# Optimization experiments

Hardware: AMD Instinct MI355X
Metric: run time of the kernel (lower is better)

## Reference

```python
import jax, jax.numpy as jnp
import numpy as np

NUM_HEADS = 8
NORM_GROUPS = 32
EPS = 1e-5


def setup_inputs() -> dict:
    key = jax.random.key(0)
    k1, k2, k3 = jax.random.split(key, 3)
    b, c, h, w = 16, 256, 64, 64
    x = jax.random.normal(k1, (b, c, h, w), dtype=jnp.float32)
    gn_w = jnp.ones((c,), dtype=jnp.float32)
    gn_b = jnp.zeros((c,), dtype=jnp.float32)
    # 1x1 convs == channel matmuls; init like torch (kaiming-ish scale)
    w_qkv = jax.random.normal(k2, (3 * c, c), dtype=jnp.float32) / np.sqrt(c)
    w_proj = jax.random.normal(k3, (c, c), dtype=jnp.float32) / np.sqrt(c)
    b_proj = jnp.zeros((c,), dtype=jnp.float32)
    return {"x": x, "gn_w": gn_w, "gn_b": gn_b, "w_qkv": w_qkv,
            "w_proj": w_proj, "b_proj": b_proj}


def reference(x, gn_w, gn_b, w_qkv, w_proj, b_proj):
    b, c, h, w = x.shape
    H = NUM_HEADS
    d = c // H
    n = h * w
    # GroupNorm over (channels_per_group, h, w)
    xg = x.reshape(b, NORM_GROUPS, -1)
    mu = jnp.mean(xg, axis=-1, keepdims=True)
    var = jnp.mean(jnp.square(xg - mu), axis=-1, keepdims=True)
    xn = ((xg - mu) * jax.lax.rsqrt(var + EPS)).reshape(b, c, h, w)
    xn = xn * gn_w[None, :, None, None] + gn_b[None, :, None, None]
    # 1x1 conv -> (b, 3c, h, w); channel layout is (qkv, heads, d)
    qkv = jnp.einsum('oc,bchw->bohw', w_qkv, xn)
    qkv = qkv.reshape(b, 3, H, d, n)
    q, k, v = qkv[:, 0], qkv[:, 1], qkv[:, 2]  # each (b, H, d, n)
    k = jax.nn.softmax(k, axis=-1)
    # linear attention: small (d x d) state per head
    att = jnp.einsum('bhdn,bhen->bhde', k, v)
    out = jnp.einsum('bhde,bhdn->bhen', att, q)  # (b, H, d, n)
    out = out.reshape(b, c, h, w)
    return jnp.einsum('oc,bchw->bohw', w_proj, out) + b_proj[None, :, None, None]
```

## Files before the change

kernel.cpp:

```cpp
#include <hip/hip_runtime.h>
#include <stdint.h>

#define BATCH 16
#define CCH   256
#define NSP   4096
#define QKV_M 768

typedef unsigned short u16;
typedef short  short8 __attribute__((ext_vector_type(8)));
typedef float  f32x4  __attribute__((ext_vector_type(4)));

__device__ __forceinline__ float bf2f(u16 h) {
  union { unsigned int u; float f; } x; x.u = ((unsigned int)h) << 16; return x.f;
}
__device__ __forceinline__ u16 f2bf(float f) {
  union { float f; unsigned int u; } x; x.f = f;
  unsigned int r = 0x7fffu + ((x.u >> 16) & 1u);
  return (u16)((x.u + r) >> 16);
}

#define GLB(p) ((__attribute__((address_space(1))) void*)(p))
#define LDSP(p) ((__attribute__((address_space(3))) void*)(p))

__global__ __launch_bounds__(256) void convw_kernel(const float* __restrict__ wq,
                                                    const float* __restrict__ wp,
                                                    u16* __restrict__ dst) {
  const int i = (blockIdx.x * 256 + threadIdx.x) * 4;
  float4 v = (i < 196608) ? *(const float4*)(wq + i)
                          : *(const float4*)(wp + (i - 196608));
  ushort4 o;
  o.x = f2bf(v.x); o.y = f2bf(v.y); o.z = f2bf(v.z); o.w = f2bf(v.w);
  *(ushort4*)(dst + i) = o;
}

__global__ __launch_bounds__(256) void gn_stats(const float* __restrict__ x,
                                                float2* __restrict__ stats,
                                                float* __restrict__ att4) {
  const int blk = blockIdx.x;
  const int tid = threadIdx.x;
  {
    float* az = att4 + (size_t)blk * 264;
    for (int i = tid; i < 264; i += 256) az[i] = 0.f;
  }
  const float4* xv = (const float4*)(x + (size_t)blk * 32768);
  float s = 0.f, ss = 0.f;
  for (int i = tid; i < 8192; i += 256) {
    float4 u = xv[i];
    s  += u.x + u.y + u.z + u.w;
    ss += u.x * u.x + u.y * u.y + u.z * u.z + u.w * u.w;
  }
#pragma unroll
  for (int off = 32; off > 0; off >>= 1) {
    s  += __shfl_down(s, off);
    ss += __shfl_down(ss, off);
  }
  __shared__ float red[8];
  const int wave = tid >> 6, lane = tid & 63;
  if (lane == 0) { red[wave * 2] = s; red[wave * 2 + 1] = ss; }
  __syncthreads();
  if (tid == 0) {
    const float S  = red[0] + red[2] + red[4] + red[6];
    const float SS = red[1] + red[3] + red[5] + red[7];
    const float mean = S * (1.f / 32768.f);
    const float var  = SS * (1.f / 32768.f) - mean * mean;
    stats[blk] = make_float2(mean, rsqrtf(var + 1e-5f));
  }
}

__global__ __launch_bounds__(256) void gn_apply_t(const float* __restrict__ x,
                                                  const float* __restrict__ gw,
                                                  const float* __restrict__ gb,
                                                  const float2* __restrict__ stats,
                                                  u16* __restrict__ xnT) {
  __shared__ u16 ls[64][72];
  const int b = blockIdx.z, c0 = blockIdx.y * 64, n0 = blockIdx.x * 64;
  const int tid = threadIdx.x;
#pragma unroll
  for (int r = 0; r < 4; ++r) {
    const int cc = (tid >> 4) + r * 16;
    const int nn = (tid & 15) * 4;
    const int c = c0 + cc;
    const float2 st = stats[b * 32 + (c >> 3)];
    const float wv = gw[c] * st.y;
    const float bv = gb[c] - st.x * wv;
    float4 u = *(const float4*)(x + ((size_t)b * CCH + c) * NSP + n0 + nn);
    ushort4 o;
    o.x = f2bf(u.x * wv + bv);
    o.y = f2bf(u.y * wv + bv);
    o.z = f2bf(u.z * wv + bv);
    o.w = f2bf(u.w * wv + bv);
    *(ushort4*)&ls[cc][nn] = o;
  }
  __syncthreads();
#pragma unroll
  for (int p = 0; p < 2; ++p) {
    const int idx = tid + p * 256;
    const int nn = idx >> 3;
    const int cb = (idx & 7) * 8;
    u16 tmp[8];
#pragma unroll
    for (int j = 0; j < 8; ++j) tmp[j] = ls[cb + j][nn];
    *(uint4*)(xnT + ((size_t)b * NSP + n0 + nn) * CCH + c0 + cb) = *(uint4*)tmp;
  }
}

template <int OUTF32, int TRQ>
__global__ __launch_bounds__(256) void gemm_mfma(const u16* __restrict__ A,
                                                 const u16* __restrict__ Bt,
                                                 const float* __restrict__ bias,
                                                 void* __restrict__ Cm, int M,
                                                 int aBatch, long btStride) {
  __shared__ __align__(16) u16 smem[17408];
  const int tid = threadIdx.x, wave = tid >> 6, lane = tid & 63;
  const int n0 = blockIdx.x * 128, m0 = blockIdx.y * 128, bz = blockIdx.z;
  const u16* Ab = A + (size_t)bz * aBatch;
  const u16* Bb = Bt + (size_t)bz * btStride;

  const int lrow = lane >> 3;
  const int kcl  = ((lane & 7) ^ lrow) * 8;
  const u16* pA[4]; const u16* pB[4];
#pragma unroll
  for (int j = 0; j < 4; ++j) {
    const int row = j * 32 + wave * 8 + lrow;
    pA[j] = Ab + (size_t)(m0 + row) * CCH + kcl;
    pB[j] = Bb + (size_t)(n0 + row) * CCH + kcl;
  }
  u16* lA = smem;
  u16* lB = smem + 8192;

  const int wm = wave >> 1, wn = wave & 1;
  f32x4 acc[4][4];
#pragma unroll
  for (int i = 0; i < 4; ++i)
#pragma unroll
    for (int j = 0; j < 4; ++j) acc[i][j] = (f32x4){0.f, 0.f, 0.f, 0.f};

  for (int it = 0; it < 4; ++it) {
#pragma unroll
    for (int j = 0; j < 4; ++j) {
      __builtin_amdgcn_global_load_lds(GLB(pA[j]), LDSP(lA + (j * 256 + wave * 64) * 8), 16, 0, 0);
      __builtin_amdgcn_global_load_lds(GLB(pB[j]), LDSP(lB + (j * 256 + wave * 64) * 8), 16, 0, 0);
      pA[j] += 64; pB[j] += 64;
    }
    __syncthreads();
#pragma unroll
    for (int w = 0; w < 2; ++w) {
      const int kcf = w * 4 + (lane >> 4);
      short8 af[4], bfr[4];
#pragma unroll
      for (int mt = 0; mt < 4; ++mt) {
        const int row = wm * 64 + mt * 16 + (lane & 15);
        af[mt] = *(const short8*)&lA[(row * 8 + (kcf ^ (row & 7))) * 8];
      }
#pragma unroll
      for (int nt = 0; nt < 4; ++nt) {
        const int row = wn * 64 + nt * 16 + (lane & 15);
        bfr[nt] = *(const short8*)&lB[(row * 8 + (kcf ^ (row & 7))) * 8];
      }
#pragma unroll
      for (int mt = 0; mt < 4; ++mt)
#pragma unroll
        for (int nt = 0; nt < 4; ++nt)
          acc[mt][nt] = __builtin_amdgcn_mfma_f32_16x16x32_bf16(af[mt], bfr[nt], acc[mt][nt], 0, 0, 0);
    }
    __syncthreads();
  }

  if (!OUTF32) {
    u16* cl = smem;
    const bool tr = TRQ && (m0 < 256);
#pragma unroll
    for (int mt = 0; mt < 4; ++mt)
#pragma unroll
      for (int nt = 0; nt < 4; ++nt)
#pragma unroll
        for (int r = 0; r < 4; ++r) {
          const int row = wm * 64 + mt * 16 + (lane >> 4) * 4 + r;
          const int col = wn * 64 + nt * 16 + (lane & 15);
          if (tr) cl[col * 136 + row] = f2bf(acc[mt][nt][r]);
          else    cl[row * 136 + col] = f2bf(acc[mt][nt][r]);
        }
    __syncthreads();
    u16* C = (u16*)Cm + (size_t)bz * M * NSP;
    if (tr) {
#pragma unroll
      for (int j = 0; j < 8; ++j) {
        const int idx = tid + j * 256;
        const int nl = idx >> 4, mc = (idx & 15) * 8;
        *(uint4*)(C + (size_t)(n0 + nl) * CCH + m0 + mc) =
            *(const uint4*)&cl[nl * 136 + mc];
      }
    } else {
#pragma unroll
      for (int j = 0; j < 8; ++j) {
        const int idx = tid + j * 256;
        const int row = idx >> 4, chunk = idx & 15;
        *(uint4*)(C + (size_t)(m0 + row) * NSP + n0 + chunk * 8) =
            *(const uint4*)&cl[row * 136 + chunk * 8];
      }
    }
  } else {
    float* clf = (float*)smem;
    float* C = (float*)Cm + (size_t)bz * M * NSP;
#pragma unroll
    for (int pass = 0; pass < 2; ++pass) {
      if (wm == pass) {
#pragma unroll
        for (int mt = 0; mt < 4; ++mt)
#pragma unroll
          for (int nt = 0; nt < 4; ++nt)
#pragma unroll
            for (int r = 0; r < 4; ++r) {
              const int rl = mt * 16 + (lane >> 4) * 4 + r;
              const int col = wn * 64 + nt * 16 + (lane & 15);
              clf[rl * 132 + col] = acc[mt][nt][r] + bias[m0 + pass * 64 + rl];
            }
      }
      __syncthreads();
#pragma unroll
      for (int j = 0; j < 8; ++j) {
        const int idx = tid + j * 256;
        const int row = idx >> 5, chunk = idx & 31;
        *(float4*)(C + (size_t)(m0 + pass * 64 + row) * NSP + n0 + chunk * 4) =
            *(const float4*)&clf[row * 132 + chunk * 4];
      }
      __syncthreads();
    }
  }
}

__global__ __launch_bounds__(256, 4) void att2_kernel(const u16* __restrict__ qkv,
                                                      float* __restrict__ att4) {
  const int b = blockIdx.z, h = blockIdx.y;
  const int bh = b * 8 + h;
  const int tid = threadIdx.x, wave = tid >> 6, lane = tid & 63;
  const int n0 = blockIdx.x * 512 + wave * 128;
  const u16* kp = qkv + ((size_t)b * QKV_M + 256 + h * 32) * NSP;
  const u16* vp = qkv + ((size_t)b * QKV_M + 512 + h * 32) * NSP;
  const int r  = lane & 15;
  const int kc = (lane >> 4) * 8;

  f32x4 acc[2][2], accl[2];
#pragma unroll
  for (int i = 0; i < 2; ++i) {
    accl[i] = (f32x4){0.f, 0.f, 0.f, 0.f};
#pragma unroll
    for (int j = 0; j < 2; ++j) acc[i][j] = (f32x4){0.f, 0.f, 0.f, 0.f};
  }
  short8 ones;
#pragma unroll
  for (int j = 0; j < 8; ++j) ones[j] = (short)0x3F80;

  const size_t base0 = (size_t)r * NSP + (size_t)(n0 + kc);
#pragma unroll
  for (int c = 0; c < 4; ++c) {
    const size_t off = base0 + (size_t)c * 32;
    short8 k0 = *(const short8*)(kp + off);
    short8 k1 = *(const short8*)(kp + off + (size_t)16 * NSP);
    short8 v0 = *(const short8*)(vp + off);
    short8 v1 = *(const short8*)(vp + off + (size_t)16 * NSP);
    short8 e0, e1;
#pragma unroll
    for (int j = 0; j < 8; ++j) {
      e0[j] = (short)f2bf(__expf(bf2f((u16)k0[j])));
      e1[j] = (short)f2bf(__expf(bf2f((u16)k1[j])));
    }
    acc[0][0] = __builtin_amdgcn_mfma_f32_16x16x32_bf16(e0, v0, acc[0][0], 0, 0, 0);
    acc[0][1] = __builtin_amdgcn_mfma_f32_16x16x32_bf16(e0, v1, acc[0][1], 0, 0, 0);
    acc[1][0] = __builtin_amdgcn_mfma_f32_16x16x32_bf16(e1, v0, acc[1][0], 0, 0, 0);
    acc[1][1] = __builtin_amdgcn_mfma_f32_16x16x32_bf16(e1, v1, acc[1][1], 0, 0, 0);
    accl[0]   = __builtin_amdgcn_mfma_f32_16x16x32_bf16(e0, ones, accl[0], 0, 0, 0);
    accl[1]   = __builtin_amdgcn_mfma_f32_16x16x32_bf16(e1, ones, accl[1], 0, 0, 0);
  }

  __shared__ float ratt[4][32][34];
  __shared__ float rl[4][32];
  const int rq = lane >> 4;
#pragma unroll
  for (int dt = 0; dt < 2; ++dt) {
#pragma unroll
    for (int et = 0; et < 2; ++et)
#pragma unroll
      for (int j = 0; j < 4; ++j)
        ratt[wave][dt * 16 + rq * 4 + j][et * 16 + r] = acc[dt][et][j];
    if (r == 0)
#pragma unroll
      for (int j = 0; j < 4; ++j) rl[wave][dt * 16 + rq * 4 + j] = accl[dt][j];
  }
  __syncthreads();
  float* ap = att4 + (size_t)bh * 1056;
  for (int i = tid; i < 1024; i += 256) {
    const int d = i >> 5, e = i & 31;
    atomicAdd(&ap[i], ratt[0][d][e] + ratt[1][d][e] + ratt[2][d][e] + ratt[3][d][e]);
  }
  if (tid < 32)
    atomicAdd(&ap[1024 + tid], rl[0][tid] + rl[1][tid] + rl[2][tid] + rl[3][tid]);
}

__global__ __launch_bounds__(256) void w2_kernel(const u16* __restrict__ wp_bf,
                                                 const float* __restrict__ att4,
                                                 u16* __restrict__ W2) {
  const int b = blockIdx.x >> 4;
  const int o0 = (blockIdx.x & 15) * 16;
  const int tid = threadIdx.x;
  const int h = tid >> 5, d = tid & 31;
  const float* ap = att4 + ((size_t)b * 8 + h) * 1056;
  const float linv = 1.f / ap[1024 + d];
  float as[32];
#pragma unroll
  for (int e = 0; e < 32; ++e) as[e] = ap[d * 32 + e] * linv;
  u16* w2p = W2 + (size_t)b * 65536;
  for (int oi = 0; oi < 16; ++oi) {
    const int o = o0 + oi;
    const uint4* wr = (const uint4*)(wp_bf + o * 256 + h * 32);
    float acc = 0.f;
#pragma unroll
    for (int j = 0; j < 4; ++j) {
      uint4 u = wr[j];
      const u16* w8 = (const u16*)&u;
#pragma unroll
      for (int t = 0; t < 8; ++t) acc += bf2f(w8[t]) * as[j * 8 + t];
    }
    w2p[o * 256 + tid] = f2bf(acc);
  }
}

extern "C" void kernel_launch(void* const* d_in, const int* in_sizes, int n_in,
                              void* d_out, int out_size, void* d_ws, size_t ws_size,
                              hipStream_t stream) {
  const float* x      = (const float*)d_in[0];
  const float* gn_w   = (const float*)d_in[1];
  const float* gn_b   = (const float*)d_in[2];
  const float* w_qkv  = (const float*)d_in[3];
  const float* w_proj = (const float*)d_in[4];
  const float* b_proj = (const float*)d_in[5];
  float* out = (float*)d_out;

  char* ws = (char*)d_ws;
  u16*    xnT   = (u16*)ws;
  u16*    qkv   = (u16*)(ws + 33554432ull);
  float*  att4  = (float*)(ws + 134217728ull);
  float2* stats = (float2*)(ws + 134758400ull);
  u16*    wbf   = (u16*)(ws + 134762496ull);
  u16* wq_bf = wbf;
  u16* wp_bf = wbf + 196608;
  u16* W2 = xnT;

  convw_kernel<<<256, 256, 0, stream>>>(w_qkv, w_proj, wbf);
  gn_stats<<<512, 256, 0, stream>>>(x, stats, att4);
  gn_apply_t<<<dim3(64, 4, 16), 256, 0, stream>>>(x, gn_w, gn_b, stats, xnT);
  gemm_mfma<0, 1><<<dim3(32, 6, 16), 256, 0, stream>>>(wq_bf, xnT, nullptr, qkv,
                                                       QKV_M, 0, (long)NSP * CCH);
  att2_kernel<<<dim3(8, 8, 16), 256, 0, stream>>>(qkv, att4);
  w2_kernel<<<256, 256, 0, stream>>>(wp_bf, att4, W2);
  gemm_mfma<1, 0><<<dim3(32, 2, 16), 256, 0, stream>>>(W2, qkv, b_proj, out,
                                                       CCH, 65536, (long)QKV_M * NSP);
}
```

Before: 234.3 us.

## Fuse K/V projection GEMM with linear-attention state accumulation

The QKV GEMM now computes only the Q rows, and a new kernel computes the K and V tiles per 128-column block directly from the normalized input. It applies exp to K, keeps both tiles in LDS, and accumulates the per-head K·V^T and softmax denominators into att4 with atomics. This avoids writing K and V to global memory and reading them back in a separate pass. In exchange, each block issues many more global atomics (32 column blocks per head instead of 8), and LDS use grows to about 68KB per block, which may lower occupancy.

```diff
diff --git a/kernel.cpp b/kernel.cpp
--- a/kernel.cpp
+++ b/kernel.cpp
@@ -229,72 +229,126 @@
   }
 }
 
-__global__ __launch_bounds__(256, 4) void att2_kernel(const u16* __restrict__ qkv,
-                                                      float* __restrict__ att4) {
-  const int b = blockIdx.z, h = blockIdx.y;
-  const int bh = b * 8 + h;
+__global__ __launch_bounds__(256) void gemm_kv_att(const u16* __restrict__ A,
+                                                   const u16* __restrict__ Bt,
+                                                   float* __restrict__ att4) {
+  __shared__ __align__(16) u16 smem[34816];
   const int tid = threadIdx.x, wave = tid >> 6, lane = tid & 63;
-  const int n0 = blockIdx.x * 512 + wave * 128;
-  const u16* kp = qkv + ((size_t)b * QKV_M + 256 + h * 32) * NSP;
-  const u16* vp = qkv + ((size_t)b * QKV_M + 512 + h * 32) * NSP;
-  const int r  = lane & 15;
-  const int kc = (lane >> 4) * 8;
-
-  f32x4 acc[2][2], accl[2];
+  const int n0 = blockIdx.x * 128, hg = blockIdx.y, b = blockIdx.z;
+  const u16* Bb = Bt + (size_t)b * (size_t)NSP * CCH;
+
+  const int lrow = lane >> 3;
+  const int kcl  = ((lane & 7) ^ lrow) * 8;
+  u16* lA  = smem;
+  u16* lB  = smem + 8192;
+  u16* clK = smem + 17408;
+  u16* clV = smem;
+  const int wm = wave >> 1, wn = wave & 1;
+
+  for (int pass = 0; pass < 2; ++pass) {
+    const int m0 = 256 + pass * 256 + hg * 128;
+    const u16* pA[4]; const u16* pB[4];
+#pragma unroll
+    for (int j = 0; j < 4; ++j) {
+      const int row = j * 32 + wave * 8 + lrow;
+      pA[j] = A  + (size_t)(m0 + row) * CCH + kcl;
+      pB[j] = Bb + (size_t)(n0 + row) * CCH + kcl;
+    }
+    f32x4 acc[4][4];
+#pragma unroll
+    for (int i = 0; i < 4; ++i)
+#pragma unroll
+      for (int j = 0; j < 4; ++j) acc[i][j] = (f32x4){0.f, 0.f, 0.f, 0.f};
+
+    for (int it = 0; it < 4; ++it) {
+#pragma unroll
+      for (int j = 0; j < 4; ++j) {
+        __builtin_amdgcn_global_load_lds(GLB(pA[j]), LDSP(lA + (j * 256 + wave * 64) * 8), 16, 0, 0);
+        __builtin_amdgcn_global_load_lds(GLB(pB[j]), LDSP(lB + (j * 256 + wave * 64) * 8), 16, 0, 0);
+        pA[j] += 64; pB[j] += 64;
+      }
+      __syncthreads();
+#pragma unroll
+      for (int w = 0; w < 2; ++w) {
+        const int kcf = w * 4 + (lane >> 4);
+        short8 af[4], bfr[4];
+#pragma unroll
+        for (int mt = 0; mt < 4; ++mt) {
+          const int row = wm * 64 + mt * 16 + (lane & 15);
+          af[mt] = *(const short8*)&lA[(row * 8 + (kcf ^ (row & 7))) * 8];
+        }
+#pragma unroll
+        for (int nt = 0; nt < 4; ++nt) {
+          const int row = wn * 64 + nt * 16 + (lane & 15);
+          bfr[nt] = *(const short8*)&lB[(row * 8 + (kcf ^ (row & 7))) * 8];
+        }
+#pragma unroll
+        for (int mt = 0; mt < 4; ++mt)
+#pragma unroll
+          for (int nt = 0; nt < 4; ++nt)
+            acc[mt][nt] = __builtin_amdgcn_mfma_f32_16x16x32_bf16(af[mt], bfr[nt], acc[mt][nt], 0, 0, 0);
+      }
+      __syncthreads();
+    }
+
+    u16* cl = pass ? clV : clK;
+#pragma unroll
+    for (int mt = 0; mt < 4; ++mt)
+#pragma unroll
+      for (int nt = 0; nt < 4; ++nt)
+#pragma unroll
+        for (int r = 0; r < 4; ++r) {
+          const int row = wm * 64 + mt * 16 + (lane >> 4) * 4 + r;
+          const int col = wn * 64 + nt * 16 + (lane & 15);
+          const float v = acc[mt][nt][r];
+          cl[row * 136 + col] = f2bf(pass ? v : __expf(v));
+        }
+  }
+  __syncthreads();
+
+  const int hh = wave;
+  const int bh = b * 8 + hg * 4 + hh;
+  f32x4 a2[2][2], al[2];
 #pragma unroll
   for (int i = 0; i < 2; ++i) {
-    accl[i] = (f32x4){0.f, 0.f, 0.f, 0.f};
-#pragma unroll
-    for (int j = 0; j < 2; ++j) acc[i][j] = (f32x4){0.f, 0.f, 0.f, 0.f};
+    al[i] = (f32x4){0.f, 0.f, 0.f, 0.f};
+#pragma unroll
+    for (int j = 0; j < 2; ++j) a2[i][j] = (f32x4){0.f, 0.f, 0.f, 0.f};
   }
   short8 ones;
 #pragma unroll
   for (int j = 0; j < 8; ++j) ones[j] = (short)0x3F80;
 
-  const size_t base0 = (size_t)r * NSP + (size_t)(n0 + kc);
+  const int rr = lane & 15, cc8 = (lane >> 4) * 8;
 #pragma unroll
   for (int c = 0; c < 4; ++c) {
-    const size_t off = base0 + (size_t)c * 32;
-    short8 k0 = *(const short8*)(kp + off);
-    short8 k1 = *(const short8*)(kp + off + (size_t)16 * NSP);
-    short8 v0 = *(const short8*)(vp + off);
-    short8 v1 = *(const short8*)(vp + off + (size_t)16 * NSP);
-    short8 e0, e1;
-#pragma unroll
-    for (int j = 0; j < 8; ++j) {
-      e0[j] = (short)f2bf(__expf(bf2f((u16)k0[j])));
-      e1[j] = (short)f2bf(__expf(bf2f((u16)k1[j])));
-    }
-    acc[0][0] = __builtin_amdgcn_mfma_f32_16x16x32_bf16(e0, v0, acc[0][0], 0, 0, 0);
-    acc[0][1] = __builtin_amdgcn_mfma_f32_16x16x32_bf16(e0, v1, acc[0][1], 0, 0, 0);
-    acc[1][0] = __builtin_amdgcn_mfma_f32_16x16x32_bf16(e1, v0, acc[1][0], 0, 0, 0);
-    acc[1][1] = __builtin_amdgcn_mfma_f32_16x16x32_bf16(e1, v1, acc[1][1], 0, 0, 0);
-    accl[0]   = __builtin_amdgcn_mfma_f32_16x16x32_bf16(e0, ones, accl[0], 0, 0, 0);
-    accl[1]   = __builtin_amdgcn_mfma_f32_16x16x32_bf16(e1, ones, accl[1], 0, 0, 0);
-  }
-
-  __shared__ float ratt[4][32][34];
-  __shared__ float rl[4][32];
-  const int rq = lane >> 4;
-#pragma unroll
-  for (int dt = 0; dt < 2; ++dt) {
-#pragma unroll
-    for (int et = 0; et < 2; ++et)
+    const int n = c * 32 + cc8;
+    short8 ek0 = *(const short8*)&clK[(hh * 32 + rr) * 136 + n];
+    short8 ek1 = *(const short8*)&clK[(hh * 32 + 16 + rr) * 136 + n];
+    short8 v0  = *(const short8*)&clV[(hh * 32 + rr) * 136 + n];
+    short8 v1  = *(const short8*)&clV[(hh * 32 + 16 + rr) * 136 + n];
+    a2[0][0] = __builtin_amdgcn_mfma_f32_16x16x32_bf16(ek0, v0, a2[0][0], 0, 0, 0);
+    a2[0][1] = __builtin_amdgcn_mfma_f32_16x16x32_bf16(ek0, v1, a2[0][1], 0, 0, 0);
+    a2[1][0] = __builtin_amdgcn_mfma_f32_16x16x32_bf16(ek1, v0, a2[1][0], 0, 0, 0);
+    a2[1][1] = __builtin_amdgcn_mfma_f32_16x16x32_bf16(ek1, v1, a2[1][1], 0, 0, 0);
+    al[0]    = __builtin_amdgcn_mfma_f32_16x16x32_bf16(ek0, ones, al[0], 0, 0, 0);
+    al[1]    = __builtin_amdgcn_mfma_f32_16x16x32_bf16(ek1, ones, al[1], 0, 0, 0);
+  }
+
+  float* ap = att4 + (size_t)bh * 1056;
+  const int dq = (lane >> 4) * 4;
+#pragma unroll
+  for (int dh = 0; dh < 2; ++dh) {
+#pragma unroll
+    for (int eh = 0; eh < 2; ++eh)
 #pragma unroll
       for (int j = 0; j < 4; ++j)
-        ratt[wave][dt * 16 + rq * 4 + j][et * 16 + r] = acc[dt][et][j];
-    if (r == 0)
-#pragma unroll
-      for (int j = 0; j < 4; ++j) rl[wave][dt * 16 + rq * 4 + j] = accl[dt][j];
-  }
-  __syncthreads();
-  float* ap = att4 + (size_t)bh * 1056;
-  for (int i = tid; i < 1024; i += 256) {
-    const int d = i >> 5, e = i & 31;
-    atomicAdd(&ap[i], ratt[0][d][e] + ratt[1][d][e] + ratt[2][d][e] + ratt[3][d][e]);
-  }
-  if (tid < 32)
-    atomicAdd(&ap[1024 + tid], rl[0][tid] + rl[1][tid] + rl[2][tid] + rl[3][tid]);
+        atomicAdd(&ap[(dh * 16 + dq + j) * 32 + eh * 16 + rr], a2[dh][eh][j]);
+    if (rr == 0)
+#pragma unroll
+      for (int j = 0; j < 4; ++j)
+        atomicAdd(&ap[1024 + dh * 16 + dq + j], al[dh][j]);
+  }
 }
 
 __global__ __launch_bounds__(256) void w2_kernel(const u16* __restrict__ wp_bf,
@@ -349,9 +403,9 @@
   convw_kernel<<<256, 256, 0, stream>>>(w_qkv, w_proj, wbf);
   gn_stats<<<512, 256, 0, stream>>>(x, stats, att4);
   gn_apply_t<<<dim3(64, 4, 16), 256, 0, stream>>>(x, gn_w, gn_b, stats, xnT);
-  gemm_mfma<0, 1><<<dim3(32, 6, 16), 256, 0, stream>>>(wq_bf, xnT, nullptr, qkv,
+  gemm_mfma<0, 1><<<dim3(32, 2, 16), 256, 0, stream>>>(wq_bf, xnT, nullptr, qkv,
                                                        QKV_M, 0, (long)NSP * CCH);
-  att2_kernel<<<dim3(8, 8, 16), 256, 0, stream>>>(qkv, att4);
+  gemm_kv_att<<<dim3(32, 2, 16), 256, 0, stream>>>(wq_bf, xnT, att4);
   w2_kernel<<<256, 256, 0, stream>>>(wp_bf, att4, W2);
   gemm_mfma<1, 0><<<dim3(32, 2, 16), 256, 0, stream>>>(W2, qkv, b_proj, out,
                                                        CCH, 65536, (long)QKV_M * NSP);
```

Result: slower. 246.9 us (+5.4%).
